# Performance work log

Measured on AMD Instinct MI355X. Metric: run time of the kernel, lower is better.

Reference implementation:

```python
import jax, jax.numpy as jnp
import numpy as np

LSTM_IN = 125
LSTM_H = 125
MLP_D_H = 512
N = 512


def _lstm_scan(x, Wih, Whh, bih, bhh):
    # x: (N, LSTM_IN); PyTorch gate order: i, f, g, o
    H = LSTM_H
    def step(carry, xt):
        h, c = carry
        g = Wih @ xt + Whh @ h + bih + bhh  # (4H,)
        i = jax.nn.sigmoid(g[:H])
        f = jax.nn.sigmoid(g[H:2 * H])
        gg = jnp.tanh(g[2 * H:3 * H])
        o = jax.nn.sigmoid(g[3 * H:])
        c = f * c + i * gg
        h = o * jnp.tanh(c)
        return (h, c), h
    init = (jnp.zeros((H,), x.dtype), jnp.zeros((H,), x.dtype))
    _, hs = jax.lax.scan(step, init, x)
    return hs  # (N, H)


def setup_inputs() -> dict:
    key = jax.random.key(0)
    ks = jax.random.split(key, 14)
    s = 0.05
    d = {
        "sentence_emb": jax.random.normal(ks[0], (N, 1, LSTM_IN), jnp.float32),
        "Wih_f": jax.random.normal(ks[1], (4 * LSTM_H, LSTM_IN), jnp.float32) * s,
        "Whh_f": jax.random.normal(ks[2], (4 * LSTM_H, LSTM_H), jnp.float32) * s,
        "bih_f": jax.random.normal(ks[3], (4 * LSTM_H,), jnp.float32) * s,
        "bhh_f": jax.random.normal(ks[4], (4 * LSTM_H,), jnp.float32) * s,
        "Wih_b": jax.random.normal(ks[5], (4 * LSTM_H, LSTM_IN), jnp.float32) * s,
        "Whh_b": jax.random.normal(ks[6], (4 * LSTM_H, LSTM_H), jnp.float32) * s,
        "bih_b": jax.random.normal(ks[7], (4 * LSTM_H,), jnp.float32) * s,
        "bhh_b": jax.random.normal(ks[8], (4 * LSTM_H,), jnp.float32) * s,
        "W1": jax.random.normal(ks[9], (MLP_D_H, 4 * LSTM_H), jnp.float32) * s,
        "b1": jax.random.normal(ks[10], (MLP_D_H,), jnp.float32) * s,
        "W2": jax.random.normal(ks[11], (1, MLP_D_H), jnp.float32) * s,
        "b2": jax.random.normal(ks[12], (1,), jnp.float32) * s,
    }
    return d


def reference(sentence_emb, Wih_f, Whh_f, bih_f, bhh_f, Wih_b, Whh_b, bih_b, bhh_b, W1, b1, W2, b2):
    x = sentence_emb[:, 0, :]  # (N, 125), batch=1
    h_fwd = _lstm_scan(x, Wih_f, Whh_f, bih_f, bhh_f)           # (N, 125)
    h_bwd = _lstm_scan(x[::-1], Wih_b, Whh_b, bih_b, bhh_b)[::-1]  # (N, 125)
    h = jnp.concatenate([h_fwd, h_bwd], axis=-1)  # (N, 250)
    # output_mtx[i, j] = MLP(concat(h[j], h[i]))
    # Decompose first linear: W1 @ cat(h_j, h_i) = Wa @ h_j + Wb @ h_i
    D = h.shape[-1]
    Pa = h @ W1[:, :D].T   # (N, H): contribution of h_j
    Pb = h @ W1[:, D:].T   # (N, H): contribution of h_i
    hidden = jnp.tanh(Pb[:, None, :] + Pa[None, :, :] + b1)  # (N, N, H)
    out = hidden @ W2[0] + b2[0]  # (N, N)
    return out
```

## Files before the change

kernel.cpp:

```cpp
#include <hip/hip_runtime.h>

typedef __bf16 bf16_t;
typedef __bf16 bf16x8 __attribute__((ext_vector_type(8)));
typedef float f32x4 __attribute__((ext_vector_type(4)));
typedef int   int4v __attribute__((ext_vector_type(4)));

#define LOG2E 1.4426950408889634f

template<int CTRL>
__device__ __forceinline__ float qperm(float x) {
  return __builtin_bit_cast(float,
      __builtin_amdgcn_update_dpp(0, __builtin_bit_cast(int, x), CTRL, 0xF, 0xF, true));
}
template<int CTRL>
__device__ __forceinline__ int qpermi(int x) {
  return __builtin_amdgcn_update_dpp(0, x, CTRL, 0xF, 0xF, true);
}

__device__ __forceinline__ void lds_barrier() {
  asm volatile("s_waitcnt lgkmcnt(0)\n\ts_barrier" ::: "memory");
}

__global__ __launch_bounds__(256) void pre_kernel(
    const float* __restrict__ x,
    const float* __restrict__ Wih_f, const float* __restrict__ bih_f,
    const float* __restrict__ bhh_f,
    const float* __restrict__ Wih_b, const float* __restrict__ bih_b,
    const float* __restrict__ bhh_b,
    float* __restrict__ preT)
{
  const int dir = blockIdx.x >> 5;
  const int T   = blockIdx.x & 31;
  const float* __restrict__ Wih = dir ? Wih_b : Wih_f;
  const float* __restrict__ bih = dir ? bih_b : bih_f;
  const float* __restrict__ bhh = dir ? bhh_b : bhh_f;

  const int tid = threadIdx.x;
  const int wv  = tid >> 6;
  const int lane = tid & 63;
  const int q = lane >> 4, cc = lane & 15;

  const int r  = 16 * T + cc;
  const int na = r >> 2, pa = r & 3;
  const bool vld = (na < 125);
  const float* __restrict__ Wr = Wih + (vld ? (125 * pa + na) * 125 : 0);

  bf16x8 whi[4], wlo[4];
  #pragma unroll
  for (int ks = 0; ks < 4; ++ks) {
    #pragma unroll
    for (int j = 0; j < 8; ++j) {
      int k = 32 * ks + 8 * q + j;
      float wvv = (vld && k < 125) ? Wr[k] : 0.0f;
      bf16_t hi = (bf16_t)wvv;
      whi[ks][j] = hi;
      wlo[ks][j] = (bf16_t)(wvv - (float)hi);
    }
  }

  float bias[4];
  #pragma unroll
  for (int reg = 0; reg < 4; ++reg) {
    int ro = 16 * T + 4 * q + reg;
    int no = ro >> 2, po = ro & 3;
    bias[reg] = (no < 125) ? (bih[125 * po + no] + bhh[125 * po + no]) : 0.0f;
  }

  for (int i = 0; i < 8; ++i) {
    const int tt = 8 * wv + i;
    const int t  = 16 * tt + cc;
    const int trow = dir ? (511 - t) : t;
    const float* __restrict__ xr = x + trow * 125;

    f32x4 acc = (f32x4)0.0f;
    #pragma unroll
    for (int ks = 0; ks < 4; ++ks) {
      bf16x8 xhi, xlo;
      #pragma unroll
      for (int j = 0; j < 8; ++j) {
        int k = 32 * ks + 8 * q + j;
        float xv = (k < 125) ? xr[k] : 0.0f;
        bf16_t hi = (bf16_t)xv;
        xhi[j] = hi;
        xlo[j] = (bf16_t)(xv - (float)hi);
      }
      acc = __builtin_amdgcn_mfma_f32_16x16x32_bf16(whi[ks], xhi, acc, 0, 0, 0);
      acc = __builtin_amdgcn_mfma_f32_16x16x32_bf16(whi[ks], xlo, acc, 0, 0, 0);
      acc = __builtin_amdgcn_mfma_f32_16x16x32_bf16(wlo[ks], xhi, acc, 0, 0, 0);
    }
    #pragma unroll
    for (int reg = 0; reg < 4; ++reg) {
      int ro = 16 * T + 4 * q + reg;
      preT[dir * 262144 + ro * 512 + 16 * tt + cc] = acc[reg] + bias[reg];
    }
  }
}

__global__ __launch_bounds__(512, 2) void lstm_kernel(
    const float* __restrict__ Whh_f, const float* __restrict__ Whh_b,
    const float* __restrict__ pre,
    bf16_t* __restrict__ h_all)
{
  const int dir = blockIdx.x;
  const float* __restrict__ Whh = dir ? Whh_b : Whh_f;

  const int tid = threadIdx.x;
  const int w   = tid >> 6;
  const int p   = tid & 3;
  const int Q   = tid >> 2;
  const bool valid = (Q < 125);

  float wm = 0.0f;
  if (valid) {
    #pragma unroll
    for (int g = 0; g < 4; ++g) {
      const float* __restrict__ Wrow = Whh + (125 * g + Q) * 125;
      #pragma unroll
      for (int kk = 0; kk < 32; ++kk) {
        int k = 32 * p + kk;
        if (k < 125) wm = fmaxf(wm, fabsf(Wrow[k]));
      }
    }
  }
  #pragma unroll
  for (int off = 1; off < 64; off <<= 1)
    wm = fmaxf(wm, __shfl_xor(wm, off));
  __shared__ float wmx[8];
  if ((tid & 63) == 0) wmx[w] = wm;
  __syncthreads();
  float wmax = wmx[0];
  #pragma unroll
  for (int u = 1; u < 8; ++u) wmax = fmaxf(wmax, wmx[u]);
  const float s_w  = 127.0f / wmax;
  const float invq = wmax / (127.0f * 127.0f);

  int wq[4][8];
  #pragma unroll
  for (int g = 0; g < 4; ++g) {
    const float* __restrict__ Wrow = Whh + (valid ? (125 * g + Q) * 125 : 0);
    #pragma unroll
    for (int d = 0; d < 8; ++d) {
      int b = 0;
      #pragma unroll
      for (int byte = 0; byte < 4; ++byte) {
        int k = 32 * p + 4 * d + byte;
        int qv = 0;
        if (valid && k < 125)
          qv = (int)__builtin_rintf(Wrow[k] * s_w);
        b |= (qv & 0xFF) << (8 * byte);
      }
      wq[g][d] = b;
    }
  }

  __shared__ __align__(16) char hbuf[2][128];
  if (tid < 256) hbuf[tid >> 7][tid & 127] = 0;
  if (dir == 0) {
    #pragma unroll
    for (int u = 0; u < 6; ++u) h_all[tid * 256 + 250 + u] = (bf16_t)0.0f;
  }
  __syncthreads();

  const float mult   = (p == 2) ? (-2.0f * LOG2E) : (-LOG2E);
  const float sA     = (p == 2) ? 2.0f : 1.0f;
  const float sB     = (p == 2) ? -1.0f : 0.0f;
  const float dscale = mult * invq;
  const float* __restrict__ preR = pre + dir * 262144 + tid * 512;
  float c = 0.0f;

  float4 pv_cur = *(const float4*)preR;

  for (int gg = 0; gg < 128; ++gg) {
    float4 pv_nxt = make_float4(0.f, 0.f, 0.f, 0.f);
    if (gg < 127) pv_nxt = *(const float4*)(preR + 4 * (gg + 1));

    #pragma unroll
    for (int s4 = 0; s4 < 4; ++s4) {
      const int step = 4 * gg + s4;
      const int cur  = s4 & 1, nxt = cur ^ 1;
      const float pv = (s4 == 0) ? pv_cur.x : (s4 == 1) ? pv_cur.y
                     : (s4 == 2) ? pv_cur.z : pv_cur.w;
      const float pvm = mult * pv;

      const int4v hv0 = *(const int4v*)&hbuf[cur][32 * p];
      const int4v hv1 = *(const int4v*)&hbuf[cur][32 * p + 16];

      int acc[4];
      #pragma unroll
      for (int g = 0; g < 4; ++g) {
        int a = 0;
        a = __builtin_amdgcn_sdot4(wq[g][0], hv0[0], a, false);
        a = __builtin_amdgcn_sdot4(wq[g][1], hv0[1], a, false);
        a = __builtin_amdgcn_sdot4(wq[g][2], hv0[2], a, false);
        a = __builtin_amdgcn_sdot4(wq[g][3], hv0[3], a, false);
        a = __builtin_amdgcn_sdot4(wq[g][4], hv1[0], a, false);
        a = __builtin_amdgcn_sdot4(wq[g][5], hv1[1], a, false);
        a = __builtin_amdgcn_sdot4(wq[g][6], hv1[2], a, false);
        a = __builtin_amdgcn_sdot4(wq[g][7], hv1[3], a, false);
        acc[g] = a;
      }

      #pragma unroll
      for (int g = 0; g < 4; ++g) {
        int s1 = acc[g] + qpermi<0xB1>(acc[g]);
        acc[g] = s1 + qpermi<0x4E>(s1);
      }
      int g01  = (p & 1) ? acc[1] : acc[0];
      int g23  = (p & 1) ? acc[3] : acc[2];
      int gsel = (p & 2) ? g23 : g01;

      float xg  = fmaf((float)gsel, dscale, pvm);
      float e   = __builtin_amdgcn_exp2f(xg);
      float y   = __builtin_amdgcn_rcpf(1.0f + e);
      float act = fmaf(y, sA, sB);

      float b_i = qperm<0x00>(act);
      float b_f = qperm<0x55>(act);
      float b_g = qperm<0xAA>(act);
      float b_o = qperm<0xFF>(act);
      c = fmaf(b_f, c, b_i * b_g);
      float e2 = __builtin_amdgcn_exp2f(-2.0f * LOG2E * c);
      float tc = fmaf(__builtin_amdgcn_rcpf(1.0f + e2), 2.0f, -1.0f);
      float h  = b_o * tc;

      if (p == 0) {
        hbuf[nxt][Q] = (char)(int)__builtin_rintf(h * 127.0f);
        if (Q < 125) {
          int t_orig = dir ? (511 - step) : step;
          h_all[t_orig * 256 + dir * 125 + Q] = (bf16_t)h;
        }
      }
      lds_barrier();
    }
    pv_cur = pv_nxt;
  }
}

__global__ __launch_bounds__(256) void qgemm_kernel(
    const bf16_t* __restrict__ h_all,
    const float* __restrict__ W1,
    const float* __restrict__ b1,
    float* __restrict__ Qa,
    float* __restrict__ Qb)
{
  const int tid  = threadIdx.x;
  const int wv   = tid >> 6;
  const int lane = tid & 63;
  const int q    = lane >> 4, cc = lane & 15;
  const int bj   = blockIdx.x & 31;
  const int bm   = blockIdx.x >> 5;
  const int m    = bm * 64 + wv * 16 + cc;
  const int j0   = bj * 16;
  const int jA   = j0 + cc;

  const bool isB = (m >= 512);
  const int  row = isB ? (m - 512) : m;
  const int  cof = isB ? 250 : 0;

  f32x4 acc = (f32x4)0.0f;
  #pragma unroll
  for (int ks = 0; ks < 8; ++ks) {
    int kb = 32 * ks + 8 * q;
    bf16x8 a = *(const bf16x8*)&h_all[jA * 256 + kb];
    bf16x8 b;
    #pragma unroll
    for (int jj = 0; jj < 8; ++jj) {
      int k = kb + jj;
      float v = (k < 250) ? W1[row * 500 + cof + k] : 0.0f;
      b[jj] = (bf16_t)v;
    }
    acc = __builtin_amdgcn_mfma_f32_16x16x32_bf16(a, b, acc, 0, 0, 0);
  }

  const float C2 = 2.0f * LOG2E;
  #pragma unroll
  for (int reg = 0; reg < 4; ++reg) {
    int j = j0 + 4 * q + reg;
    float v = acc[reg];
    if (!isB) Qa[j * 512 + m] = C2 * v;
    else      Qb[j * 512 + (m - 512)] = C2 * (v + b1[m - 512]);
  }
}

__global__ __launch_bounds__(256) void outer_kernel(
    const float* __restrict__ Qa, const float* __restrict__ Qb,
    const float* __restrict__ W2, const float* __restrict__ b2,
    float* __restrict__ out)
{
  __shared__ float sa[2][32][33];
  __shared__ float sb[2][32][33];
  __shared__ float sw[2][32];

  const int tid  = threadIdx.x;
  const int bk   = blockIdx.x >> 8;
  const int tile = blockIdx.x & 255;
  const int bi   = tile >> 4, bjx = tile & 15;
  const int i0   = bi * 32, j0 = bjx * 32;
  const int ii0  = (tid & 15) * 2;
  const int jj0  = (tid >> 4) * 2;
  const int ljj  = tid & 31, kk4 = (tid >> 5) * 4;
  const int kbase = bk * 256;

  float accR[2][2] = {{0.0f, 0.0f}, {0.0f, 0.0f}};
  float wsum = 0.0f;

  for (int kc = 0; kc < 8; ++kc) {
    const int buf = kc & 1;
    const int k0  = kbase + kc * 32;
    float4 va = *(const float4*)&Qa[(j0 + ljj) * 512 + k0 + kk4];
    float4 vb = *(const float4*)&Qb[(i0 + ljj) * 512 + k0 + kk4];
    sa[buf][kk4 + 0][ljj] = va.x; sa[buf][kk4 + 1][ljj] = va.y;
    sa[buf][kk4 + 2][ljj] = va.z; sa[buf][kk4 + 3][ljj] = va.w;
    sb[buf][kk4 + 0][ljj] = vb.x; sb[buf][kk4 + 1][ljj] = vb.y;
    sb[buf][kk4 + 2][ljj] = vb.z; sb[buf][kk4 + 3][ljj] = vb.w;
    if (tid < 32) sw[buf][tid] = W2[k0 + tid];
    __syncthreads();

    #pragma unroll 4
    for (int kk = 0; kk < 32; ++kk) {
      float2 av = *(const float2*)&sa[buf][kk][jj0];
      float2 bv = *(const float2*)&sb[buf][kk][ii0];
      float wk = sw[buf][kk];
      wsum += wk;
      {
        float e = __builtin_amdgcn_exp2f(av.x + bv.x);
        accR[0][0] = fmaf(wk, __builtin_amdgcn_rcpf(1.0f + e), accR[0][0]);
      }
      {
        float e = __builtin_amdgcn_exp2f(av.y + bv.x);
        accR[0][1] = fmaf(wk, __builtin_amdgcn_rcpf(1.0f + e), accR[0][1]);
      }
      {
        float e = __builtin_amdgcn_exp2f(av.x + bv.y);
        accR[1][0] = fmaf(wk, __builtin_amdgcn_rcpf(1.0f + e), accR[1][0]);
      }
      {
        float e = __builtin_amdgcn_exp2f(av.y + bv.y);
        accR[1][1] = fmaf(wk, __builtin_amdgcn_rcpf(1.0f + e), accR[1][1]);
      }
    }
  }

  const float bb = (bk == 0) ? b2[0] : 0.0f;
  #pragma unroll
  for (int i2 = 0; i2 < 2; ++i2)
    #pragma unroll
    for (int j2 = 0; j2 < 2; ++j2)
      atomicAdd(&out[(i0 + ii0 + i2) * 512 + (j0 + jj0 + j2)],
                wsum - 2.0f * accR[i2][j2] + bb);
}

extern "C" void kernel_launch(void* const* d_in, const int* in_sizes, int n_in,
                              void* d_out, int out_size, void* d_ws, size_t ws_size,
                              hipStream_t stream) {
  const float* emb   = (const float*)d_in[0];
  const float* Wih_f = (const float*)d_in[1];
  const float* Whh_f = (const float*)d_in[2];
  const float* bih_f = (const float*)d_in[3];
  const float* bhh_f = (const float*)d_in[4];
  const float* Wih_b = (const float*)d_in[5];
  const float* Whh_b = (const float*)d_in[6];
  const float* bih_b = (const float*)d_in[7];
  const float* bhh_b = (const float*)d_in[8];
  const float* W1    = (const float*)d_in[9];
  const float* b1    = (const float*)d_in[10];
  const float* W2    = (const float*)d_in[11];
  const float* b2    = (const float*)d_in[12];
  float* out = (float*)d_out;

  char* ws = (char*)d_ws;
  float*  pre   = (float*)ws;
  bf16_t* h_all = (bf16_t*)(ws + 2 * 1024 * 1024);
  float*  Qa    = (float*)(ws + 2 * 1024 * 1024 + 256 * 1024);
  float*  Qb    = Qa + 512 * 512;

  pre_kernel<<<64, 256, 0, stream>>>(emb, Wih_f, bih_f, bhh_f,
                                     Wih_b, bih_b, bhh_b, pre);
  lstm_kernel<<<2, 512, 0, stream>>>(Whh_f, Whh_b, pre, h_all);
  qgemm_kernel<<<512, 256, 0, stream>>>(h_all, W1, b1, Qa, Qb);
  hipMemsetAsync(out, 0, (size_t)out_size * sizeof(float), stream);
  outer_kernel<<<512, 256, 0, stream>>>(Qa, Qb, W2, b2, out);
}
```

Baseline: 363.3 us.

## Merge both LSTM directions into one block, prescale pre-activations, fuse output zeroing

Runs the forward and backward LSTM recurrences in a single 1024-thread block on one CU, each direction with its own LDS h buffer, instead of two 512-thread blocks. The per-gate exp2 multiplier is folded into the stored pre-activations, removing a multiply from the serial loop. The hipMemsetAsync of the output is replaced by zeroing inside qgemm_kernel, which drops one launch. Because the two directions now share every barrier, one direction can stall the other, and placing both on a single CU may slow the per-step latency.

```diff
diff --git a/kernel.cpp b/kernel.cpp
--- a/kernel.cpp
+++ b/kernel.cpp
@@ -91,23 +91,24 @@
     #pragma unroll
     for (int reg = 0; reg < 4; ++reg) {
       int ro = 16 * T + 4 * q + reg;
-      preT[dir * 262144 + ro * 512 + 16 * tt + cc] = acc[reg] + bias[reg];
-    }
-  }
-}
-
-__global__ __launch_bounds__(512, 2) void lstm_kernel(
+      const float multp = (reg == 2) ? (-2.0f * LOG2E) : (-LOG2E);
+      preT[dir * 262144 + ro * 512 + 16 * tt + cc] = multp * (acc[reg] + bias[reg]);
+    }
+  }
+}
+
+__global__ __launch_bounds__(1024, 4) void lstm_kernel(
     const float* __restrict__ Whh_f, const float* __restrict__ Whh_b,
     const float* __restrict__ pre,
     bf16_t* __restrict__ h_all)
 {
-  const int dir = blockIdx.x;
+  const int tid = threadIdx.x;
+  const int dir = tid >> 9;
   const float* __restrict__ Whh = dir ? Whh_b : Whh_f;
 
-  const int tid = threadIdx.x;
   const int w   = tid >> 6;
   const int p   = tid & 3;
-  const int Q   = tid >> 2;
+  const int Q   = (tid >> 2) & 127;
   const bool valid = (Q < 125);
 
   float wm = 0.0f;
@@ -125,12 +126,12 @@
   #pragma unroll
   for (int off = 1; off < 64; off <<= 1)
     wm = fmaxf(wm, __shfl_xor(wm, off));
-  __shared__ float wmx[8];
+  __shared__ float wmx[16];
   if ((tid & 63) == 0) wmx[w] = wm;
   __syncthreads();
   float wmax = wmx[0];
   #pragma unroll
-  for (int u = 1; u < 8; ++u) wmax = fmaxf(wmax, wmx[u]);
+  for (int u = 1; u < 16; ++u) wmax = fmaxf(wmax, wmx[u]);
   const float s_w  = 127.0f / wmax;
   const float invq = wmax / (127.0f * 127.0f);
 
@@ -153,9 +154,9 @@
     }
   }
 
-  __shared__ __align__(16) char hbuf[2][128];
-  if (tid < 256) hbuf[tid >> 7][tid & 127] = 0;
-  if (dir == 0) {
+  __shared__ __align__(16) char hbuf[2][2][128];
+  if (tid < 512) ((char*)hbuf)[tid] = 0;
+  if (tid < 512) {
     #pragma unroll
     for (int u = 0; u < 6; ++u) h_all[tid * 256 + 250 + u] = (bf16_t)0.0f;
   }
@@ -165,7 +166,7 @@
   const float sA     = (p == 2) ? 2.0f : 1.0f;
   const float sB     = (p == 2) ? -1.0f : 0.0f;
   const float dscale = mult * invq;
-  const float* __restrict__ preR = pre + dir * 262144 + tid * 512;
+  const float* __restrict__ preR = pre + dir * 262144 + (tid & 511) * 512;
   float c = 0.0f;
 
   float4 pv_cur = *(const float4*)preR;
@@ -180,10 +181,9 @@
       const int cur  = s4 & 1, nxt = cur ^ 1;
       const float pv = (s4 == 0) ? pv_cur.x : (s4 == 1) ? pv_cur.y
                      : (s4 == 2) ? pv_cur.z : pv_cur.w;
-      const float pvm = mult * pv;
-
-      const int4v hv0 = *(const int4v*)&hbuf[cur][32 * p];
-      const int4v hv1 = *(const int4v*)&hbuf[cur][32 * p + 16];
+
+      const int4v hv0 = *(const int4v*)&hbuf[dir][cur][32 * p];
+      const int4v hv1 = *(const int4v*)&hbuf[dir][cur][32 * p + 16];
 
       int acc[4];
       #pragma unroll
@@ -209,7 +209,7 @@
       int g23  = (p & 1) ? acc[3] : acc[2];
       int gsel = (p & 2) ? g23 : g01;
 
-      float xg  = fmaf((float)gsel, dscale, pvm);
+      float xg  = fmaf((float)gsel, dscale, pv);
       float e   = __builtin_amdgcn_exp2f(xg);
       float y   = __builtin_amdgcn_rcpf(1.0f + e);
       float act = fmaf(y, sA, sB);
@@ -224,7 +224,7 @@
       float h  = b_o * tc;
 
       if (p == 0) {
-        hbuf[nxt][Q] = (char)(int)__builtin_rintf(h * 127.0f);
+        hbuf[dir][nxt][Q] = (char)(int)__builtin_rintf(h * 127.0f);
         if (Q < 125) {
           int t_orig = dir ? (511 - step) : step;
           h_all[t_orig * 256 + dir * 125 + Q] = (bf16_t)h;
@@ -241,7 +241,8 @@
     const float* __restrict__ W1,
     const float* __restrict__ b1,
     float* __restrict__ Qa,
-    float* __restrict__ Qb)
+    float* __restrict__ Qb,
+    float* __restrict__ out)
 {
   const int tid  = threadIdx.x;
   const int wv   = tid >> 6;
@@ -252,6 +253,9 @@
   const int m    = bm * 64 + wv * 16 + cc;
   const int j0   = bj * 16;
   const int jA   = j0 + cc;
+
+  out[blockIdx.x * 512 + tid]       = 0.0f;
+  out[blockIdx.x * 512 + tid + 256] = 0.0f;
 
   const bool isB = (m >= 512);
   const int  row = isB ? (m - 512) : m;
@@ -376,8 +380,7 @@
 
   pre_kernel<<<64, 256, 0, stream>>>(emb, Wih_f, bih_f, bhh_f,
                                      Wih_b, bih_b, bhh_b, pre);
-  lstm_kernel<<<2, 512, 0, stream>>>(Whh_f, Whh_b, pre, h_all);
-  qgemm_kernel<<<512, 256, 0, stream>>>(h_all, W1, b1, Qa, Qb);
-  hipMemsetAsync(out, 0, (size_t)out_size * sizeof(float), stream);
+  lstm_kernel<<<1, 1024, 0, stream>>>(Whh_f, Whh_b, pre, h_all);
+  qgemm_kernel<<<512, 256, 0, stream>>>(h_all, W1, b1, Qa, Qb, out);
   outer_kernel<<<512, 256, 0, stream>>>(Qa, Qb, W2, b2, out);
 }
```

Result: slower. 535.3 us (+47.3%).
